# Optimization experiments

Measured on AMD Instinct MI355X. Metric: run time of the kernel, lower is better.

The kernel has to match this reference:

```python
import jax, jax.numpy as jnp
import numpy as np

B, N, IN_F, OUT_F, H = 4, 2048, 128, 128, 4
D = OUT_F // H  # head_dim = 32
NEG_SLOPE = 0.2


def setup_inputs() -> dict:
    key = jax.random.key(0)
    k1, k2, k3, k4, k5 = jax.random.split(key, 5)
    x = jax.random.normal(k1, (B, N, IN_F), dtype=jnp.float32)
    adj = jax.random.randint(k2, (N, N), 0, 2, dtype=jnp.int32)
    adj = adj.at[jnp.arange(N), jnp.arange(N)].set(1)  # self-loops
    # xavier-uniform-like init
    lim_w = float(np.sqrt(6.0 / (IN_F + OUT_F)))
    W = jax.random.uniform(k3, (OUT_F, IN_F), minval=-lim_w, maxval=lim_w, dtype=jnp.float32)
    lim_a = float(np.sqrt(6.0 / (H + D)))
    a_src = jax.random.uniform(k4, (H, D), minval=-lim_a, maxval=lim_a, dtype=jnp.float32)
    a_dst = jax.random.uniform(k5, (H, D), minval=-lim_a, maxval=lim_a, dtype=jnp.float32)
    return {"x": x, "adj": adj, "W": W, "a_src": a_src, "a_dst": a_dst}


def reference(x, adj, W, a_src, a_dst):
    Bx, Nx, _ = x.shape
    # linear projection: (B,N,out) -> (B,N,H,D)
    h = jnp.einsum('bni,oi->bno', x, W).reshape(Bx, Nx, H, D)
    e_src = jnp.einsum('bnhd,hd->bnh', h, a_src)  # (B,N,H)
    e_dst = jnp.einsum('bnhd,hd->bnh', h, a_dst)  # (B,N,H)
    # scores: (B,N_src,H,N_dst)
    scores = jax.nn.leaky_relu(
        e_src[:, :, :, None] + e_dst.transpose(0, 2, 1)[:, None, :, :],
        negative_slope=NEG_SLOPE,
    )
    mask = adj[None, :, None, :]  # (1,N,1,N)
    scores = jnp.where(mask == 0, -jnp.inf, scores)
    attn = jax.nn.softmax(scores, axis=-1)  # (B,N,H,N); dropout is identity at eval
    out = jnp.einsum('bnhm,bmhd->bnhd', attn, h)  # (B,N,H,D)
    return out.reshape(Bx, Nx, H * D)
```

## Files before the change

kernel.cpp:

```cpp
#include <hip/hip_runtime.h>
#include <math.h>

#define BB 4
#define NN 2048
#define FF 128
#define HH 4
#define DD 32
#define NEG_SLOPE 0.2f
#define LOG2E 1.4426950408889634f

typedef __attribute__((ext_vector_type(8))) short short8;
typedef __attribute__((ext_vector_type(4))) float floatx4;
typedef __attribute__((ext_vector_type(2))) float floatx2;

__device__ __forceinline__ float exp2_fast(float x) {
#if __has_builtin(__builtin_amdgcn_exp2f)
    return __builtin_amdgcn_exp2f(x);
#else
    return exp2f(x);
#endif
}

__device__ __forceinline__ int bit_mask(unsigned int w, int bit) {
#if __has_builtin(__builtin_amdgcn_sbfe)
    return __builtin_amdgcn_sbfe((int)w, bit, 1);
#else
    return ((int)(w << (31 - bit))) >> 31;
#endif
}

__device__ __forceinline__ unsigned short to_bf16(float f) {
    unsigned int ui = __float_as_uint(f);
    ui += 0x7FFFu + ((ui >> 16) & 1u);
    return (unsigned short)(ui >> 16);
}

__device__ __forceinline__ unsigned int pack_pair(float e) {
    unsigned int p = to_bf16(exp2_fast(e));
    unsigned int n = to_bf16(exp2_fast(NEG_SLOPE * e));
    return (p << 16) | n;
}

__global__ __launch_bounds__(128) void k_prep(const float* __restrict__ x,
                                              const float* __restrict__ W,
                                              const float* __restrict__ a_src,
                                              const float* __restrict__ a_dst,
                                              const int* __restrict__ adj,
                                              unsigned short* __restrict__ ht,
                                              float* __restrict__ es_t,
                                              float* __restrict__ ed_t,
                                              unsigned int* __restrict__ bits) {
    __shared__ float xs[16][132];
    __shared__ float wb[128][36];
    __shared__ float as_s[FF], ad_s[FF];
    __shared__ unsigned short tile2[16][136];
    int t = threadIdx.x;

    if (blockIdx.x >= 512) {
        int idx = (blockIdx.x - 512) * 128 + t;
        int n = idx >> 6, w = idx & 63;
        const int4* base = (const int4*)(adj + (size_t)n * NN + w * 32);
        unsigned int word = 0;
#pragma unroll
        for (int q = 0; q < 8; ++q) {
            int4 a = base[q];
            word |= ((unsigned int)(a.x & 1)) << (q * 4 + 0);
            word |= ((unsigned int)(a.y & 1)) << (q * 4 + 1);
            word |= ((unsigned int)(a.z & 1)) << (q * 4 + 2);
            word |= ((unsigned int)(a.w & 1)) << (q * 4 + 3);
        }
        bits[idx] = word;
        return;
    }

    long rows0 = (long)blockIdx.x * 16;
    as_s[t] = a_src[t]; ad_s[t] = a_dst[t];
#pragma unroll
    for (int k = 0; k < 4; ++k) {
        int idx = t + k * 128;
        int r = idx >> 5, f4 = idx & 31;
        float4 v = ((const float4*)(x + (rows0 + r) * FF))[f4];
        *(float4*)&xs[r][f4 * 4] = v;
    }
    int og = t & 31, rg = t >> 5;
    float acc[4][4];
#pragma unroll
    for (int a = 0; a < 4; ++a)
#pragma unroll
        for (int c = 0; c < 4; ++c) acc[a][c] = 0.f;

    for (int c4 = 0; c4 < 4; ++c4) {
        __syncthreads();
#pragma unroll
        for (int k = 0; k < 8; ++k) {
            int idx = t + k * 128;
            int wr = idx >> 3, f4 = idx & 7;
            float4 v = *(const float4*)(W + (long)wr * FF + c4 * 32 + f4 * 4);
            *(float4*)&wb[wr][f4 * 4] = v;
        }
        __syncthreads();
#pragma unroll
        for (int ii = 0; ii < 8; ++ii) {
            int i = ii * 4;
            float4 xv[4], wv[4];
#pragma unroll
            for (int a = 0; a < 4; ++a)
                xv[a] = *(const float4*)&xs[rg * 4 + a][c4 * 32 + i];
#pragma unroll
            for (int c = 0; c < 4; ++c)
                wv[c] = *(const float4*)&wb[og * 4 + c][i];
#pragma unroll
            for (int a = 0; a < 4; ++a)
#pragma unroll
                for (int c = 0; c < 4; ++c) {
                    acc[a][c] += xv[a].x * wv[c].x + xv[a].y * wv[c].y
                               + xv[a].z * wv[c].z + xv[a].w * wv[c].w;
                }
        }
    }

    int head = og >> 3;
    int b = (int)(rows0 >> 11);
    int m_block = (int)(rows0 & 2047);
    float es[4], ed[4];
#pragma unroll
    for (int a = 0; a < 4; ++a) {
        float s = 0.f, d = 0.f;
#pragma unroll
        for (int c = 0; c < 4; ++c) {
            int col = og * 4 + c;
            s += acc[a][c] * as_s[col];
            d += acc[a][c] * ad_s[col];
        }
        es[a] = s; ed[a] = d;
    }
#pragma unroll
    for (int k = 1; k < 8; k <<= 1) {
#pragma unroll
        for (int a = 0; a < 4; ++a) {
            es[a] += __shfl_xor(es[a], k);
            ed[a] += __shfl_xor(ed[a], k);
        }
    }
    if ((og & 7) == 0) {
        size_t eb = (size_t)(b * HH + head) * NN + m_block + rg * 4;
#pragma unroll
        for (int a = 0; a < 4; ++a) {
            es_t[eb + a] = es[a] * LOG2E;
            ed_t[eb + a] = ed[a] * LOG2E;
        }
    }

#pragma unroll
    for (int a = 0; a < 4; ++a)
#pragma unroll
        for (int c = 0; c < 4; ++c)
            tile2[rg * 4 + a][og * 4 + c] = to_bf16(acc[a][c]);
    __syncthreads();
    {
        int col = t;
        int hd = col >> 5, d = col & 31;
        unsigned short* op = ht + ((size_t)(b * HH + hd) * DD + d) * NN + m_block;
#pragma unroll
        for (int h2 = 0; h2 < 2; ++h2) {
            unsigned short tmp[8];
#pragma unroll
            for (int j = 0; j < 8; ++j) tmp[j] = tile2[h2 * 8 + j][col];
            *(int4*)(op + h2 * 8) = *(const int4*)tmp;
        }
    }
}

#define HBS 1032
__global__ __launch_bounds__(512) void k_attn(
        const unsigned short* __restrict__ ht,
        const unsigned int* __restrict__ bits,
        const float* __restrict__ es_t,
        const float* __restrict__ ed_t,
        float* __restrict__ out) {
    __shared__ unsigned short hb[DD * HBS];
    __shared__ unsigned int epk[NN];
    int t = threadIdx.x;
    int n0 = blockIdx.x * 64;
    int bh = blockIdx.y;
    int b = bh >> 2, head = bh & 3;

    int wid = t >> 6, lane = t & 63;
    int q = lane >> 4, r = lane & 15;
    int qo = q * 8;
    int ks = wid >> 2, rg2 = wid & 3;
    int n_row = n0 + rg2 * 16 + r;

    {
        float4 v = ((const float4*)(ed_t + (size_t)bh * NN))[t];
        uint4 o = {pack_pair(v.x), pack_pair(v.y), pack_pair(v.z), pack_pair(v.w)};
        ((uint4*)epk)[t] = o;
    }
    int4 bw[8];
    {
        const int4* bp0 = (const int4*)(bits + (size_t)n_row * 64 + ks * 16);
        const int4* bp1 = (const int4*)(bits + (size_t)n_row * 64 + 32 + ks * 16);
#pragma unroll
        for (int g = 0; g < 4; ++g) { bw[g] = bp0[g]; bw[4 + g] = bp1[g]; }
    }
    float esv = es_t[(size_t)bh * NN + n_row];
    floatx2 es2 = {exp2_fast(esv), exp2_fast(NEG_SLOPE * esv)};

    floatx4 acc0 = {0.f, 0.f, 0.f, 0.f};
    floatx4 acc1 = {0.f, 0.f, 0.f, 0.f};
    floatx4 accd = {0.f, 0.f, 0.f, 0.f};
    union { short8 s8; int i[4]; } ones;
    ones.i[0] = 0x3F803F80; ones.i[1] = 0x3F803F80;
    ones.i[2] = 0x3F803F80; ones.i[3] = 0x3F803F80;

    const unsigned short* htp = ht + (size_t)bh * DD * NN;

    for (int half = 0; half < 2; ++half) {
        __syncthreads();
#pragma unroll
        for (int k = 0; k < 8; ++k) {
            int qq = t + k * 512;
            int d = qq >> 7, cm = qq & 127;
            int4 v = *(const int4*)(htp + (size_t)d * NN + half * 1024 + cm * 8);
            *(int4*)&hb[d * HBS + cm * 8] = v;
        }
        __syncthreads();
        const unsigned int* pq = epk + half * 1024 + ks * 512;
        const unsigned short* h0 = &hb[r * HBS + ks * 512 + qo];
        const unsigned short* h1 = &hb[(16 + r) * HBS + ks * 512 + qo];
        int bbase = half * 4;

#pragma unroll
        for (int it = 0; it < 16; ++it) {
            unsigned int word = (unsigned int)((&bw[bbase + (it >> 2)].x)[it & 3]);
            int mb = it * 32;
            unsigned int wq = word >> qo;
            uint4 u0 = *(const uint4*)(pq + mb + qo);
            uint4 u1 = *(const uint4*)(pq + mb + qo + 4);
            union { short8 s8; int i[4]; } af;
#pragma unroll
            for (int jp = 0; jp < 4; ++jp) {
                unsigned int c0 = (jp < 2) ? (&u0.x)[jp * 2]     : (&u1.x)[(jp - 2) * 2];
                unsigned int c1 = (jp < 2) ? (&u0.x)[jp * 2 + 1] : (&u1.x)[(jp - 2) * 2 + 1];
                floatx2 d0 = {__uint_as_float(c0 & 0xFFFF0000u),
                              __uint_as_float(c0 << 16)};
                floatx2 d1 = {__uint_as_float(c1 & 0xFFFF0000u),
                              __uint_as_float(c1 << 16)};
                floatx2 p0 = es2 * d0;
                floatx2 p1 = es2 * d1;
                float w0 = fmaxf(p0.x, p0.y);
                float w1 = fmaxf(p1.x, p1.y);
                int m0 = bit_mask(wq, 2 * jp);
                int m1 = bit_mask(wq, 2 * jp + 1);
                w0 = __uint_as_float(__float_as_uint(w0) & (unsigned int)m0);
                w1 = __uint_as_float(__float_as_uint(w1) & (unsigned int)m1);
                af.i[jp] = __builtin_amdgcn_perm(__float_as_uint(w1),
                                                 __float_as_uint(w0),
                                                 0x07060302u);
            }
            short8 b0 = *(const short8*)(h0 + mb);
            short8 b1 = *(const short8*)(h1 + mb);
            acc0 = __builtin_amdgcn_mfma_f32_16x16x32_bf16(af.s8, b0, acc0, 0, 0, 0);
            acc1 = __builtin_amdgcn_mfma_f32_16x16x32_bf16(af.s8, b1, acc1, 0, 0, 0);
            accd = __builtin_amdgcn_mfma_f32_16x16x32_bf16(af.s8, ones.s8, accd, 0, 0, 0);
        }
    }

    __syncthreads();
    float* scr = (float*)hb;
    if (ks == 1) {
        int base = (rg2 * 64 + lane) * 12;
        *(floatx4*)&scr[base + 0] = acc0;
        *(floatx4*)&scr[base + 4] = acc1;
        *(floatx4*)&scr[base + 8] = accd;
    }
    __syncthreads();
    if (ks == 0) {
        int base = (rg2 * 64 + lane) * 12;
        floatx4 p0 = *(const floatx4*)&scr[base + 0];
        floatx4 p1 = *(const floatx4*)&scr[base + 4];
        floatx4 pd = *(const floatx4*)&scr[base + 8];
#pragma unroll
        for (int k = 0; k < 4; ++k) {
            acc0[k] += p0[k]; acc1[k] += p1[k]; accd[k] += pd[k];
        }
#pragma unroll
        for (int reg = 0; reg < 4; ++reg) {
            int nrow = n0 + rg2 * 16 + q * 4 + reg;
            float inv = 1.0f / accd[reg];
            float* op = out + ((size_t)(b * NN + nrow)) * FF + head * DD;
            op[r]      = acc0[reg] * inv;
            op[16 + r] = acc1[reg] * inv;
        }
    }
}

extern "C" void kernel_launch(void* const* d_in, const int* in_sizes, int n_in,
                              void* d_out, int out_size, void* d_ws, size_t ws_size,
                              hipStream_t stream) {
    const float* x     = (const float*)d_in[0];
    const int*   adj   = (const int*)d_in[1];
    const float* W     = (const float*)d_in[2];
    const float* a_src = (const float*)d_in[3];
    const float* a_dst = (const float*)d_in[4];
    float* out = (float*)d_out;

    float* es_t = (float*)d_ws;
    float* ed_t = es_t + (size_t)BB * HH * NN;
    unsigned int* bits = (unsigned int*)(ed_t + (size_t)BB * HH * NN);
    unsigned short* ht = (unsigned short*)(bits + (size_t)NN * (NN / 32));

    hipLaunchKernelGGL(k_prep, dim3(1536), dim3(128), 0, stream,
                       x, W, a_src, a_dst, adj, ht, es_t, ed_t, bits);
    hipLaunchKernelGGL(k_attn, dim3(NN / 64, BB * HH), dim3(512), 0, stream,
                       ht, bits, es_t, ed_t, out);
}
```

Measured before the change: 116.5 us.

## Stage full head value tile once per 128-row block with 1024-thread attention

The attention kernel now handles 128 query rows per block with 1024 threads. It loads the whole 32x2048 bf16 value tile into LDS in a single stage instead of two halves with extra barriers, and each set of 8 waves covers half of the key range. The exp2 destination terms are stored as fp32 pairs instead of packed bf16, which removes unpacking ALU work but doubles LDS reads for those terms. LDS use rises to about 148 KB per block, so only one block fits per CU and there are half as many blocks, which may reduce latency hiding and load overlap.

```diff
diff --git a/kernel.cpp b/kernel.cpp
--- a/kernel.cpp
+++ b/kernel.cpp
@@ -33,12 +33,6 @@
     unsigned int ui = __float_as_uint(f);
     ui += 0x7FFFu + ((ui >> 16) & 1u);
     return (unsigned short)(ui >> 16);
-}
-
-__device__ __forceinline__ unsigned int pack_pair(float e) {
-    unsigned int p = to_bf16(exp2_fast(e));
-    unsigned int n = to_bf16(exp2_fast(NEG_SLOPE * e));
-    return (p << 16) | n;
 }
 
 __global__ __launch_bounds__(128) void k_prep(const float* __restrict__ x,
@@ -171,40 +165,52 @@
     }
 }
 
-#define HBS 1032
-__global__ __launch_bounds__(512) void k_attn(
+#define HTS 2056
+__global__ __launch_bounds__(1024) void k_attn(
         const unsigned short* __restrict__ ht,
         const unsigned int* __restrict__ bits,
         const float* __restrict__ es_t,
         const float* __restrict__ ed_t,
         float* __restrict__ out) {
-    __shared__ unsigned short hb[DD * HBS];
-    __shared__ unsigned int epk[NN];
+    __shared__ unsigned short hb[DD * HTS];
+    __shared__ float ep[NN * 2];
     int t = threadIdx.x;
-    int n0 = blockIdx.x * 64;
+    int n0 = blockIdx.x * 128;
     int bh = blockIdx.y;
     int b = bh >> 2, head = bh & 3;
 
     int wid = t >> 6, lane = t & 63;
     int q = lane >> 4, r = lane & 15;
     int qo = q * 8;
-    int ks = wid >> 2, rg2 = wid & 3;
-    int n_row = n0 + rg2 * 16 + r;
+    int half = wid >> 3, wsub = wid & 7;
+    int n_l = wsub * 16 + r;
 
     {
-        float4 v = ((const float4*)(ed_t + (size_t)bh * NN))[t];
-        uint4 o = {pack_pair(v.x), pack_pair(v.y), pack_pair(v.z), pack_pair(v.w)};
-        ((uint4*)epk)[t] = o;
+        float2 v = ((const float2*)(ed_t + (size_t)bh * NN))[t];
+        float4 o;
+        o.x = exp2_fast(v.x); o.y = exp2_fast(NEG_SLOPE * v.x);
+        o.z = exp2_fast(v.y); o.w = exp2_fast(NEG_SLOPE * v.y);
+        ((float4*)ep)[t] = o;
+    }
+    {
+        const unsigned short* htp = ht + (size_t)bh * DD * NN;
+#pragma unroll
+        for (int k = 0; k < 8; ++k) {
+            int qq = t + k * 1024;
+            int d = qq >> 8, cm = qq & 255;
+            int4 v = *(const int4*)(htp + (size_t)d * NN + cm * 8);
+            *(int4*)&hb[d * HTS + cm * 8] = v;
+        }
     }
     int4 bw[8];
     {
-        const int4* bp0 = (const int4*)(bits + (size_t)n_row * 64 + ks * 16);
-        const int4* bp1 = (const int4*)(bits + (size_t)n_row * 64 + 32 + ks * 16);
-#pragma unroll
-        for (int g = 0; g < 4; ++g) { bw[g] = bp0[g]; bw[4 + g] = bp1[g]; }
-    }
-    float esv = es_t[(size_t)bh * NN + n_row];
+        const int4* bp = (const int4*)(bits + (size_t)(n0 + n_l) * 64 + half * 32);
+#pragma unroll
+        for (int g = 0; g < 8; ++g) bw[g] = bp[g];
+    }
+    float esv = es_t[(size_t)bh * NN + n0 + n_l];
     floatx2 es2 = {exp2_fast(esv), exp2_fast(NEG_SLOPE * esv)};
+    __syncthreads();
 
     floatx4 acc0 = {0.f, 0.f, 0.f, 0.f};
     floatx4 acc1 = {0.f, 0.f, 0.f, 0.f};
@@ -213,41 +219,24 @@
     ones.i[0] = 0x3F803F80; ones.i[1] = 0x3F803F80;
     ones.i[2] = 0x3F803F80; ones.i[3] = 0x3F803F80;
 
-    const unsigned short* htp = ht + (size_t)bh * DD * NN;
-
-    for (int half = 0; half < 2; ++half) {
-        __syncthreads();
-#pragma unroll
-        for (int k = 0; k < 8; ++k) {
-            int qq = t + k * 512;
-            int d = qq >> 7, cm = qq & 127;
-            int4 v = *(const int4*)(htp + (size_t)d * NN + half * 1024 + cm * 8);
-            *(int4*)&hb[d * HBS + cm * 8] = v;
-        }
-        __syncthreads();
-        const unsigned int* pq = epk + half * 1024 + ks * 512;
-        const unsigned short* h0 = &hb[r * HBS + ks * 512 + qo];
-        const unsigned short* h1 = &hb[(16 + r) * HBS + ks * 512 + qo];
-        int bbase = half * 4;
-
-#pragma unroll
-        for (int it = 0; it < 16; ++it) {
-            unsigned int word = (unsigned int)((&bw[bbase + (it >> 2)].x)[it & 3]);
-            int mb = it * 32;
+    const float* eph = ep + half * 2048;
+    const unsigned short* hrow0 = &hb[r * HTS + half * 1024 + qo];
+    const unsigned short* hrow1 = hrow0 + 16 * HTS;
+
+#pragma unroll
+    for (int g = 0; g < 8; ++g) {
+#pragma unroll
+        for (int c = 0; c < 4; ++c) {
+            unsigned int word = (unsigned int)((&bw[g].x)[c]);
+            int mb = (g * 4 + c) * 32;
             unsigned int wq = word >> qo;
-            uint4 u0 = *(const uint4*)(pq + mb + qo);
-            uint4 u1 = *(const uint4*)(pq + mb + qo + 4);
+            const float* pbase = eph + (mb + qo) * 2;
             union { short8 s8; int i[4]; } af;
 #pragma unroll
             for (int jp = 0; jp < 4; ++jp) {
-                unsigned int c0 = (jp < 2) ? (&u0.x)[jp * 2]     : (&u1.x)[(jp - 2) * 2];
-                unsigned int c1 = (jp < 2) ? (&u0.x)[jp * 2 + 1] : (&u1.x)[(jp - 2) * 2 + 1];
-                floatx2 d0 = {__uint_as_float(c0 & 0xFFFF0000u),
-                              __uint_as_float(c0 << 16)};
-                floatx2 d1 = {__uint_as_float(c1 & 0xFFFF0000u),
-                              __uint_as_float(c1 << 16)};
-                floatx2 p0 = es2 * d0;
-                floatx2 p1 = es2 * d1;
+                float4 d2 = *(const float4*)(pbase + jp * 4);
+                floatx2 p0 = es2 * (floatx2){d2.x, d2.y};
+                floatx2 p1 = es2 * (floatx2){d2.z, d2.w};
                 float w0 = fmaxf(p0.x, p0.y);
                 float w1 = fmaxf(p1.x, p1.y);
                 int m0 = bit_mask(wq, 2 * jp);
@@ -258,8 +247,8 @@
                                                  __float_as_uint(w0),
                                                  0x07060302u);
             }
-            short8 b0 = *(const short8*)(h0 + mb);
-            short8 b1 = *(const short8*)(h1 + mb);
+            short8 b0 = *(const short8*)(hrow0 + mb);
+            short8 b1 = *(const short8*)(hrow1 + mb);
             acc0 = __builtin_amdgcn_mfma_f32_16x16x32_bf16(af.s8, b0, acc0, 0, 0, 0);
             acc1 = __builtin_amdgcn_mfma_f32_16x16x32_bf16(af.s8, b1, acc1, 0, 0, 0);
             accd = __builtin_amdgcn_mfma_f32_16x16x32_bf16(af.s8, ones.s8, accd, 0, 0, 0);
@@ -268,15 +257,15 @@
 
     __syncthreads();
     float* scr = (float*)hb;
-    if (ks == 1) {
-        int base = (rg2 * 64 + lane) * 12;
+    if (wid >= 8) {
+        int base = ((wid - 8) * 64 + lane) * 12;
         *(floatx4*)&scr[base + 0] = acc0;
         *(floatx4*)&scr[base + 4] = acc1;
         *(floatx4*)&scr[base + 8] = accd;
     }
     __syncthreads();
-    if (ks == 0) {
-        int base = (rg2 * 64 + lane) * 12;
+    if (wid < 8) {
+        int base = (wid * 64 + lane) * 12;
         floatx4 p0 = *(const floatx4*)&scr[base + 0];
         floatx4 p1 = *(const floatx4*)&scr[base + 4];
         floatx4 pd = *(const floatx4*)&scr[base + 8];
@@ -286,7 +275,7 @@
         }
 #pragma unroll
         for (int reg = 0; reg < 4; ++reg) {
-            int nrow = n0 + rg2 * 16 + q * 4 + reg;
+            int nrow = n0 + wsub * 16 + q * 4 + reg;
             float inv = 1.0f / accd[reg];
             float* op = out + ((size_t)(b * NN + nrow)) * FF + head * DD;
             op[r]      = acc0[reg] * inv;
@@ -312,6 +301,6 @@
 
     hipLaunchKernelGGL(k_prep, dim3(1536), dim3(128), 0, stream,
                        x, W, a_src, a_dst, adj, ht, es_t, ed_t, bits);
-    hipLaunchKernelGGL(k_attn, dim3(NN / 64, BB * HH), dim3(512), 0, stream,
+    hipLaunchKernelGGL(k_attn, dim3(NN / 128, BB * HH), dim3(1024), 0, stream,
                        ht, bits, es_t, ed_t, out);
 }
```

Result: faster. 108.3 us (-7.1%).
